# Performance work log

Measured on AMD Instinct MI355X. Metric: run time of the kernel, lower is better.

## Reference

```python
import jax, jax.numpy as jnp
import numpy as np

N = 8192        # number of cells/nodes
D_IN = 30       # input feature dim
P_DIM = 3       # position dim
HID = 32        # attention hidden dim
D_OUT = 30      # backbone output dim
FF = 128        # MLP hidden width
SIGMA = 0.3     # spatial decay sigma


def setup_inputs() -> dict:
    key = jax.random.key(0)
    ks = jax.random.split(key, 12)
    w = lambda k, shape: (jax.random.normal(k, shape, jnp.float32) * 0.1)
    return {
        "t": jax.random.uniform(ks[0], (1,), jnp.float32),
        "Z": jax.random.normal(ks[1], (N, D_IN + P_DIM + 1), jnp.float32),
        # SpatialAttentionLayer params (Q/K/V projections + output proj)
        "Wq": w(ks[2], (D_IN, HID)), "bq": jnp.zeros((HID,), jnp.float32),
        "Wk": w(ks[3], (D_IN, HID)), "bk": jnp.zeros((HID,), jnp.float32),
        "Wv": w(ks[4], (D_IN, HID)), "bv": jnp.zeros((HID,), jnp.float32),
        "Wo": w(ks[5], (HID, D_OUT)), "bo": jnp.zeros((D_OUT,), jnp.float32),
        # LayerNorm
        "ln_g": jnp.ones((D_OUT,), jnp.float32), "ln_b": jnp.zeros((D_OUT,), jnp.float32),
        # backbone MLP: Linear(30,128) -> SiLU -> Linear(128,30)
        "W1": w(ks[6], (D_OUT, FF)), "b1": jnp.zeros((FF,), jnp.float32),
        "W2": w(ks[7], (FF, D_OUT)), "b2": jnp.zeros((D_OUT,), jnp.float32),
        # expr_head: Linear(30,30)
        "We": w(ks[8], (D_OUT, D_OUT)), "be": jnp.zeros((D_OUT,), jnp.float32),
    }


def reference(t, Z, Wq, bq, Wk, bk, Wv, bv, Wo, bo, ln_g, ln_b, W1, b1, W2, b2, We, be):
    # Z: (N, D_IN + P_DIM + 1); last column is kinetic energy (unused in fwd)
    X = Z[:, :-1]                       # (N, 33)
    P = X[:, -P_DIM:]                   # (N, 3) positions
    F = X[:, :D_IN]                     # (N, 30) features

    # --- SpatialAttentionLayer: sigma distance-decay attention, no softmax ---
    Q = F @ Wq + bq
    K = F @ Wk + bk
    V = F @ Wv + bv
    scores = (Q @ K.T) / jnp.sqrt(jnp.float32(HID))          # (N, N)
    pn = jnp.sum(P * P, axis=1)
    d2 = jnp.maximum(pn[:, None] + pn[None, :] - 2.0 * (P @ P.T), 0.0)
    decay = jnp.exp(-d2 / (2.0 * SIGMA * SIGMA))              # spatial decay kernel
    A = jax.nn.sigmoid(scores) * decay                        # no-softmax attention
    A = A / (jnp.sum(A, axis=1, keepdims=True) + 1e-8)        # row-normalized message passing
    H = (A @ V) @ Wo + bo                                     # (N, D_OUT)

    # --- LayerNorm(output_dim) ---
    mu = jnp.mean(H, axis=-1, keepdims=True)
    var = jnp.mean((H - mu) ** 2, axis=-1, keepdims=True)
    Hn = (H - mu) * jax.lax.rsqrt(var + 1e-5) * ln_g + ln_b

    # --- Linear(30,128) -> SiLU -> Linear(128,30) ---
    H2 = jax.nn.silu(Hn @ W1 + b1) @ W2 + b2

    # --- expr_head ---
    feature_velo = H2 @ We + be                               # (N, 30)

    # static_pos=True -> zero position velocities (velocity_head bypassed)
    pos_velo = jnp.zeros_like(P)                              # (N, 3)

    # kinetic energy term
    ke = 0.5 * jnp.mean(feature_velo ** 2, axis=1) + 0.5 * jnp.mean(pos_velo ** 2, axis=1)
    return jnp.concatenate([feature_velo, pos_velo, ke[:, None]], axis=1)  # (N, 34)
```

## Files before the change

kernel.cpp:

```cpp
#include <hip/hip_runtime.h>
#include <hip/hip_bf16.h>

#define N      8192
#define D_IN   30
#define HID    32
#define D_OUT  30
#define FFD    128
#define ZC     34

typedef __attribute__((ext_vector_type(8))) short short8;
typedef __attribute__((ext_vector_type(16))) float f32x16;
typedef __attribute__((ext_vector_type(2))) float f32x2;

static __device__ __forceinline__ ushort f2bf(float x) {
    uint32_t u = __float_as_uint(x);
    uint32_t r = (u + 0x7fffu + ((u >> 16) & 1u)) >> 16;
    return (ushort)r;
}
static __device__ __forceinline__ float bf2f(ushort u) {
    return __uint_as_float(((uint32_t)u) << 16);
}

__global__ __launch_bounds__(256) void dv_qkv_kernel(
    const float* __restrict__ Z,
    const float* __restrict__ Wq, const float* __restrict__ bq,
    const float* __restrict__ Wk, const float* __restrict__ bk,
    const float* __restrict__ Wv, const float* __restrict__ bv,
    const float* __restrict__ W2, const float* __restrict__ We,
    const float* __restrict__ b2, const float* __restrict__ be,
    ushort* __restrict__ Qb, ushort* __restrict__ Kb,
    ushort* __restrict__ Vt, ushort* __restrict__ KA,
    ushort* __restrict__ QB, float* __restrict__ W2e, float* __restrict__ b2e)
{
    __shared__ ushort sv[8][33];
    const int t = blockIdx.x * 256 + threadIdx.x;
    const int i = t >> 5;
    const int h = t & 31;
    const float* z = Z + (size_t)i * ZC;

    float q = bq[h], k = bk[h], v = bv[h];
#pragma unroll
    for (int d = 0; d < D_IN; ++d) {
        float zf = z[d];
        q = fmaf(zf, Wq[d * HID + h], q);
        k = fmaf(zf, Wk[d * HID + h], k);
        v = fmaf(zf, Wv[d * HID + h], v);
    }
    const float QS = 0.17677669529663687f * 1.4426950408889634f;
    Qb[(size_t)i * HID + h] = f2bf(q * QS);
    Kb[(size_t)i * HID + h] = f2bf(k);
    sv[threadIdx.x >> 5][h] = f2bf(v);

    if (h == 0) {
        float p0 = z[D_IN], p1 = z[D_IN + 1], p2 = z[D_IN + 2];
        const float C2 = 1.4426950408889634f / 0.18f;
        const float SC = sqrtf(2.0f * C2);
        float px = p0 * SC, py = p1 * SC, pz = p2 * SC;
        float w  = -C2 * (p0 * p0 + p1 * p1 + p2 * p2);
        ushort phx = f2bf(px), phy = f2bf(py), phz = f2bf(pz);
        ushort plx = f2bf(px - bf2f(phx));
        ushort ply = f2bf(py - bf2f(phy));
        ushort plz = f2bf(pz - bf2f(phz));
        ushort wh  = f2bf(w);
        ushort wl  = f2bf(w - bf2f(wh));
        const ushort one = 0x3F80;
        ushort ka0[8] = {wh, wl, one, one, phx, phy, phz, phx};
        ushort ka1[8] = {phy, phz, plx, ply, plz, plx, ply, plz};
        ushort qb0[8] = {one, one, wh, wl, phx, phy, phz, plx};
        ushort qb1[8] = {ply, plz, phx, phy, phz, plx, ply, plz};
        *(uint4*)&KA[(size_t)i * 8]           = *(uint4*)ka0;
        *(uint4*)&KA[((size_t)N + i) * 8]     = *(uint4*)ka1;
        *(uint4*)&QB[(size_t)i * 8]           = *(uint4*)qb0;
        *(uint4*)&QB[((size_t)N + i) * 8]     = *(uint4*)qb1;
    }

    if (blockIdx.x < 15) {
        int idx = blockIdx.x * 256 + threadIdx.x;
        int f = idx / 30, o = idx - f * 30;
        float acc = 0.f;
#pragma unroll
        for (int d = 0; d < D_OUT; ++d)
            acc = fmaf(W2[f * D_OUT + d], We[d * D_OUT + o], acc);
        W2e[idx] = acc;
        if (idx < D_OUT) {
            float a2 = be[idx];
#pragma unroll
            for (int d = 0; d < D_OUT; ++d)
                a2 = fmaf(b2[d], We[d * D_OUT + idx], a2);
            b2e[idx] = a2;
        }
    }

    __syncthreads();
    const int ho = threadIdx.x >> 3, io = threadIdx.x & 7;
    const int i0 = blockIdx.x * 8;
    Vt[(size_t)ho * N + i0 + io] = sv[io][ho];
}

__global__ __launch_bounds__(256, 2) void dv_attn_kernel(
    const ushort* __restrict__ Qb, const ushort* __restrict__ Kb,
    const ushort* __restrict__ Vt, const ushort* __restrict__ KA,
    const ushort* __restrict__ QB, float* __restrict__ partial, int nch)
{
    __shared__ ushort lK[128 * 32];
    __shared__ ushort lV[32 * 128];
    __shared__ ushort lKA[2][128 * 8];

    const int tid  = threadIdx.x;
    const int lane = tid & 63;
    const int wv   = tid >> 6;
    const int h2   = lane >> 5;
    const int l31  = lane & 31;
    const int rb   = blockIdx.x & 63;
    const int jg   = blockIdx.x >> 6;
    const int i0w  = rb * 128 + wv * 32;

    const ushort* qp = Qb + (size_t)(i0w + l31) * HID + h2 * 8;
    const short8 qf0 = *(const short8*)qp;
    const short8 qf1 = *(const short8*)(qp + 16);
    const short8 qaug = *(const short8*)&QB[((size_t)h2 * N + i0w + l31) * 8];

    f32x16 zacc, oacc;
#pragma unroll
    for (int r = 0; r < 16; ++r) { zacc[r] = 0.f; oacc[r] = 0.f; }
    float ssA = 0.f, ssB = 0.f;

    const int cA0 = (h2 + (l31 >> 1)) & 3;
    const int cA1 = (cA0 + 2) & 3;

    for (int ch = 0; ch < nch; ++ch) {
        const int j0 = (jg * nch + ch) << 7;
        __syncthreads();
        {
            int idx = tid;
#pragma unroll
            for (int rep = 0; rep < 2; ++rep, idx += 256) {
                int jr = idx >> 2, c = idx & 3;
                int c2 = (c + (jr >> 1)) & 3;
                *(uint4*)&lK[jr * 32 + c2 * 8] =
                    *(const uint4*)&Kb[(size_t)(j0 + jr) * HID + c * 8];
            }
            idx = tid;
#pragma unroll
            for (int rep = 0; rep < 4; ++rep, idx += 256) {
                int hh = idx >> 5, cc = idx & 31;
                int cs = cc ^ hh;
                *(uint2*)&lV[hh * 128 + cs * 4] =
                    *(const uint2*)&Vt[(size_t)hh * N + j0 + cc * 4];
            }
            {
                int half = tid >> 7, jj = tid & 127;
                *(uint4*)&lKA[half][jj * 8] =
                    *(const uint4*)&KA[((size_t)half * N + j0 + jj) * 8];
            }
        }
        __syncthreads();

#pragma unroll
        for (int t32 = 0; t32 < 4; ++t32) {
            const ushort* krow = &lK[(t32 * 32 + l31) * 32];
            short8 kf0 = *(const short8*)&krow[cA0 * 8];
            short8 kf1 = *(const short8*)&krow[cA1 * 8];
            f32x16 s = __builtin_amdgcn_mfma_f32_32x32x16_bf16(kf0, qf0, zacc, 0, 0, 0);
            s = __builtin_amdgcn_mfma_f32_32x32x16_bf16(kf1, qf1, s, 0, 0, 0);

            short8 kaug = *(const short8*)&lKA[h2][(t32 * 32 + l31) * 8];
            f32x16 gA = __builtin_amdgcn_mfma_f32_32x32x16_bf16(kaug, qaug, zacc, 0, 0, 0);

            uint32_t pk[8];
#pragma unroll
            for (int p = 0; p < 8; ++p) {
                float g0 = fminf(gA[2 * p], 0.f);
                float g1 = fminf(gA[2 * p + 1], 0.f);
                float eg0 = __builtin_amdgcn_exp2f(g0);
                float es0 = __builtin_amdgcn_exp2f(-s[2 * p]);
                float a0  = eg0 * __builtin_amdgcn_rcpf(1.0f + es0);
                float eg1 = __builtin_amdgcn_exp2f(g1);
                float es1 = __builtin_amdgcn_exp2f(-s[2 * p + 1]);
                float a1  = eg1 * __builtin_amdgcn_rcpf(1.0f + es1);
                ssA += a0;
                ssB += a1;
                asm("v_cvt_pk_bf16_f32 %0, %1, %2" : "=v"(pk[p]) : "v"(a0), "v"(a1));
            }
            union BV { uint32_t u[4]; short8 v; };
            BV fa, fb;
            fa.u[0] = pk[0]; fa.u[1] = pk[1]; fa.u[2] = pk[2]; fa.u[3] = pk[3];
            fb.u[0] = pk[4]; fb.u[1] = pk[5]; fb.u[2] = pk[6]; fb.u[3] = pk[7];

            const ushort* vrow = &lV[l31 * 128];
            const int cb = t32 * 8 + h2;
            BV b0, b1;
            *(uint2*)&b0.u[0] = *(const uint2*)&vrow[((cb    ) ^ l31) * 4];
            *(uint2*)&b0.u[2] = *(const uint2*)&vrow[((cb + 2) ^ l31) * 4];
            *(uint2*)&b1.u[0] = *(const uint2*)&vrow[((cb + 4) ^ l31) * 4];
            *(uint2*)&b1.u[2] = *(const uint2*)&vrow[((cb + 6) ^ l31) * 4];

            oacc = __builtin_amdgcn_mfma_f32_32x32x16_bf16(fa.v, b0.v, oacc, 0, 0, 0);
            oacc = __builtin_amdgcn_mfma_f32_32x32x16_bf16(fb.v, b1.v, oacc, 0, 0, 0);
        }
    }

    float ssum = ssA + ssB;
    float sst = ssum + __shfl_xor(ssum, 32, 64);
    const size_t pbase = (size_t)jg * N * 33;
    if (lane < 32)
        partial[pbase + (size_t)(i0w + lane) * 33 + 32] = sst;
#pragma unroll
    for (int r = 0; r < 16; ++r) {
        int ir = (r & 3) + 8 * (r >> 2) + 4 * h2 + i0w;
        partial[pbase + (size_t)ir * 33 + l31] = oacc[r];
    }
}

__global__ __launch_bounds__(256) void dv_epilogue_kernel(
    const float* __restrict__ partial, int JG,
    const float* __restrict__ Wo, const float* __restrict__ bo,
    const float* __restrict__ ln_g, const float* __restrict__ ln_b,
    const float* __restrict__ W1, const float* __restrict__ b1,
    const float* __restrict__ W2e, const float* __restrict__ b2e,
    float* __restrict__ out)
{
    __shared__ float sr [33 * 16];
    __shared__ float sHl[30 * 16];
    __shared__ float sHn[30 * 16];
    __shared__ float shf[128 * 16];
    __shared__ float sker[16 * 16];

    const int tid  = threadIdx.x;
    const int row0 = blockIdx.x * 16;

    for (int idx = tid; idx < 33 * 16; idx += 256) {
        int r = idx / 33, c = idx - r * 33;
        const float* pp = partial + (size_t)(row0 + r) * 33 + c;
        float s = 0.f;
#pragma unroll 4
        for (int jg = 0; jg < JG; ++jg)
            s += pp[(size_t)jg * N * 33];
        sr[c * 16 + r] = s;
    }
    __syncthreads();

    const int rl  = tid & 15, grp = tid >> 4;
    const int o0  = grp * 2;
    const bool g15 = grp < 15;

    if (g15) {
        float a0 = 0.f, a1 = 0.f;
#pragma unroll
        for (int h = 0; h < HID; ++h) {
            float2 w = *(const float2*)&Wo[h * D_OUT + o0];
            float sc = sr[h * 16 + rl];
            a0 = fmaf(sc, w.x, a0); a1 = fmaf(sc, w.y, a1);
        }
        float inv = __builtin_amdgcn_rcpf(sr[32 * 16 + rl] + 1e-8f);
        float2 bb = *(const float2*)&bo[o0];
        sHl[(o0    ) * 16 + rl] = fmaf(a0, inv, bb.x);
        sHl[(o0 + 1) * 16 + rl] = fmaf(a1, inv, bb.y);
    }
    __syncthreads();

    if (tid < 16) {
        const int r = tid;
        float mu = 0.f;
#pragma unroll
        for (int o = 0; o < D_OUT; ++o) mu += sHl[o * 16 + r];
        mu *= (1.0f / D_OUT);
        float var = 0.f;
#pragma unroll
        for (int o = 0; o < D_OUT; ++o) {
            float d = sHl[o * 16 + r] - mu; var = fmaf(d, d, var);
        }
        float rs = rsqrtf(var * (1.0f / D_OUT) + 1e-5f);
#pragma unroll
        for (int o = 0; o < D_OUT; ++o)
            sHn[o * 16 + r] = fmaf((sHl[o * 16 + r] - mu) * rs, ln_g[o], ln_b[o]);
    }
    __syncthreads();

    {
        const int f0 = grp * 8;
        float acc[8];
        float4 b4a = *(const float4*)&b1[f0];
        float4 b4b = *(const float4*)&b1[f0 + 4];
        acc[0] = b4a.x; acc[1] = b4a.y; acc[2] = b4a.z; acc[3] = b4a.w;
        acc[4] = b4b.x; acc[5] = b4b.y; acc[6] = b4b.z; acc[7] = b4b.w;
#pragma unroll
        for (int o = 0; o < D_OUT; ++o) {
            float4 wa = *(const float4*)&W1[o * FFD + f0];
            float4 wb = *(const float4*)&W1[o * FFD + f0 + 4];
            float hn = sHn[o * 16 + rl];
            acc[0] = fmaf(hn, wa.x, acc[0]); acc[1] = fmaf(hn, wa.y, acc[1]);
            acc[2] = fmaf(hn, wa.z, acc[2]); acc[3] = fmaf(hn, wa.w, acc[3]);
            acc[4] = fmaf(hn, wb.x, acc[4]); acc[5] = fmaf(hn, wb.y, acc[5]);
            acc[6] = fmaf(hn, wb.z, acc[6]); acc[7] = fmaf(hn, wb.w, acc[7]);
        }
        const float L2E = 1.4426950408889634f;
#pragma unroll
        for (int ff = 0; ff < 8; ++ff) {
            float a = acc[ff];
            shf[(f0 + ff) * 16 + rl] =
                a * __builtin_amdgcn_rcpf(1.0f + __builtin_amdgcn_exp2f(-a * L2E));
        }
    }
    __syncthreads();

    if (g15) {
        float2 bb = *(const float2*)&b2e[o0];
        float a0 = bb.x, a1 = bb.y;
#pragma unroll 8
        for (int f = 0; f < FFD; ++f) {
            float2 w = *(const float2*)&W2e[f * D_OUT + o0];
            float hf = shf[f * 16 + rl];
            a0 = fmaf(hf, w.x, a0); a1 = fmaf(hf, w.y, a1);
        }
        float* op = out + (size_t)(row0 + rl) * ZC;
        op[o0] = a0; op[o0 + 1] = a1;
        sker[grp * 16 + rl] = fmaf(a0, a0, a1 * a1);
    }
    __syncthreads();

    if (tid < 16) {
        float ke = 0.f;
#pragma unroll
        for (int g = 0; g < 15; ++g) ke += sker[g * 16 + tid];
        float* op = out + (size_t)(row0 + tid) * ZC;
        op[30] = 0.f; op[31] = 0.f; op[32] = 0.f;
        op[33] = ke * (0.5f / D_OUT);
    }
}

extern "C" void kernel_launch(void* const* d_in, const int* in_sizes, int n_in,
                              void* d_out, int out_size, void* d_ws, size_t ws_size,
                              hipStream_t stream)
{
    const float* Z  = (const float*)d_in[1];
    const float* Wq = (const float*)d_in[2];
    const float* bq = (const float*)d_in[3];
    const float* Wk = (const float*)d_in[4];
    const float* bk = (const float*)d_in[5];
    const float* Wv = (const float*)d_in[6];
    const float* bv = (const float*)d_in[7];
    const float* Wo = (const float*)d_in[8];
    const float* bo = (const float*)d_in[9];
    const float* lg = (const float*)d_in[10];
    const float* lb = (const float*)d_in[11];
    const float* W1 = (const float*)d_in[12];
    const float* b1 = (const float*)d_in[13];
    const float* W2 = (const float*)d_in[14];
    const float* b2 = (const float*)d_in[15];
    const float* We = (const float*)d_in[16];
    const float* be = (const float*)d_in[17];
    float* out = (float*)d_out;

    ushort* Qb = (ushort*)d_ws;
    ushort* Kb = Qb + (size_t)N * HID;
    ushort* Vt = Kb + (size_t)N * HID;
    ushort* KA = Vt + (size_t)N * HID;
    ushort* QB = KA + (size_t)N * 16;
    float* W2e = (float*)(QB + (size_t)N * 16);
    float* b2e = W2e + FFD * D_OUT;
    float* partial = b2e + 32;

    size_t base_bytes = (size_t)((char*)partial - (char*)d_ws);
    int JG = 16;
    while (JG > 1 && base_bytes + (size_t)JG * N * 33 * 4 > ws_size) JG >>= 1;
    int nch = N / (JG * 128);

    hipLaunchKernelGGL(dv_qkv_kernel, dim3((N * HID) / 256), dim3(256), 0, stream,
                       Z, Wq, bq, Wk, bk, Wv, bv, W2, We, b2, be,
                       Qb, Kb, Vt, KA, QB, W2e, b2e);
    hipLaunchKernelGGL(dv_attn_kernel, dim3(64 * JG), dim3(256), 0, stream,
                       Qb, Kb, Vt, KA, QB, partial, nch);
    hipLaunchKernelGGL(dv_epilogue_kernel, dim3(N / 16), dim3(256), 0, stream,
                       partial, JG, Wo, bo, lg, lb, W1, b1, W2e, b2e, out);
}
```

Before: 66.85 us.

## Fold Wo into V and compute row sums via a ones column in the MFMA

The QKV kernel now precomputes V·Wo (30 columns) plus a constant ones column, stored transposed as bf16. The attention kernel therefore gets the row-normalizer from the matrix product and drops its per-element scalar sum accumulation. The partial buffer is laid out row-major with JG contiguous, which makes the epilogue reduction coalesced and removes the Wo matmul there. The decay sign is folded into the augmented K operand. Row sums now come from bf16-rounded A values, and JG is fixed at 16 with no check against workspace size.

```diff
diff --git a/kernel.cpp b/kernel.cpp
--- a/kernel.cpp
+++ b/kernel.cpp
@@ -7,10 +7,10 @@
 #define D_OUT  30
 #define FFD    128
 #define ZC     34
+#define JGC    16
 
 typedef __attribute__((ext_vector_type(8))) short short8;
 typedef __attribute__((ext_vector_type(16))) float f32x16;
-typedef __attribute__((ext_vector_type(2))) float f32x2;
 
 static __device__ __forceinline__ ushort f2bf(float x) {
     uint32_t u = __float_as_uint(x);
@@ -26,10 +26,11 @@
     const float* __restrict__ Wq, const float* __restrict__ bq,
     const float* __restrict__ Wk, const float* __restrict__ bk,
     const float* __restrict__ Wv, const float* __restrict__ bv,
+    const float* __restrict__ Wo,
     const float* __restrict__ W2, const float* __restrict__ We,
     const float* __restrict__ b2, const float* __restrict__ be,
     ushort* __restrict__ Qb, ushort* __restrict__ Kb,
-    ushort* __restrict__ Vt, ushort* __restrict__ KA,
+    ushort* __restrict__ VWot, ushort* __restrict__ KA,
     ushort* __restrict__ QB, float* __restrict__ W2e, float* __restrict__ b2e)
 {
     __shared__ ushort sv[8][33];
@@ -63,15 +64,18 @@
         ushort plz = f2bf(pz - bf2f(phz));
         ushort wh  = f2bf(w);
         ushort wl  = f2bf(w - bf2f(wh));
-        const ushort one = 0x3F80;
-        ushort ka0[8] = {wh, wl, one, one, phx, phy, phz, phx};
-        ushort ka1[8] = {phy, phz, plx, ply, plz, plx, ply, plz};
+        ushort nhx = phx ^ 0x8000, nhy = phy ^ 0x8000, nhz = phz ^ 0x8000;
+        ushort nlx = plx ^ 0x8000, nly = ply ^ 0x8000, nlz = plz ^ 0x8000;
+        ushort nwh = wh ^ 0x8000,  nwl = wl ^ 0x8000;
+        const ushort one = 0x3F80, none = 0xBF80;
+        ushort ka0[8] = {nwh, nwl, none, none, nhx, nhy, nhz, nhx};
+        ushort ka1[8] = {nhy, nhz, nlx, nly, nlz, nlx, nly, nlz};
         ushort qb0[8] = {one, one, wh, wl, phx, phy, phz, plx};
         ushort qb1[8] = {ply, plz, phx, phy, phz, plx, ply, plz};
-        *(uint4*)&KA[(size_t)i * 8]           = *(uint4*)ka0;
-        *(uint4*)&KA[((size_t)N + i) * 8]     = *(uint4*)ka1;
-        *(uint4*)&QB[(size_t)i * 8]           = *(uint4*)qb0;
-        *(uint4*)&QB[((size_t)N + i) * 8]     = *(uint4*)qb1;
+        *(uint4*)&KA[(size_t)i * 8]       = *(uint4*)ka0;
+        *(uint4*)&KA[((size_t)N + i) * 8] = *(uint4*)ka1;
+        *(uint4*)&QB[(size_t)i * 8]       = *(uint4*)qb0;
+        *(uint4*)&QB[((size_t)N + i) * 8] = *(uint4*)qb1;
     }
 
     if (blockIdx.x < 15) {
@@ -92,14 +96,24 @@
     }
 
     __syncthreads();
-    const int ho = threadIdx.x >> 3, io = threadIdx.x & 7;
-    const int i0 = blockIdx.x * 8;
-    Vt[(size_t)ho * N + i0 + io] = sv[io][ho];
+    const int io = threadIdx.x >> 5, c = threadIdx.x & 31;
+    const int ii = blockIdx.x * 8 + io;
+    float val;
+    if (c < 30) {
+        float acc = 0.f;
+#pragma unroll
+        for (int hh = 0; hh < HID; ++hh)
+            acc = fmaf(bf2f(sv[io][hh]), Wo[hh * D_OUT + c], acc);
+        val = acc;
+    } else {
+        val = (c == 31) ? 1.0f : 0.f;
+    }
+    VWot[(size_t)c * N + ii] = f2bf(val);
 }
 
 __global__ __launch_bounds__(256, 2) void dv_attn_kernel(
     const ushort* __restrict__ Qb, const ushort* __restrict__ Kb,
-    const ushort* __restrict__ Vt, const ushort* __restrict__ KA,
+    const ushort* __restrict__ VWot, const ushort* __restrict__ KA,
     const ushort* __restrict__ QB, float* __restrict__ partial, int nch)
 {
     __shared__ ushort lK[128 * 32];
@@ -123,7 +137,6 @@
     f32x16 zacc, oacc;
 #pragma unroll
     for (int r = 0; r < 16; ++r) { zacc[r] = 0.f; oacc[r] = 0.f; }
-    float ssA = 0.f, ssB = 0.f;
 
     const int cA0 = (h2 + (l31 >> 1)) & 3;
     const int cA1 = (cA0 + 2) & 3;
@@ -135,10 +148,10 @@
             int idx = tid;
 #pragma unroll
             for (int rep = 0; rep < 2; ++rep, idx += 256) {
-                int jr = idx >> 2, c = idx & 3;
-                int c2 = (c + (jr >> 1)) & 3;
+                int jr = idx >> 2, cc = idx & 3;
+                int c2 = (cc + (jr >> 1)) & 3;
                 *(uint4*)&lK[jr * 32 + c2 * 8] =
-                    *(const uint4*)&Kb[(size_t)(j0 + jr) * HID + c * 8];
+                    *(const uint4*)&Kb[(size_t)(j0 + jr) * HID + cc * 8];
             }
             idx = tid;
 #pragma unroll
@@ -146,7 +159,7 @@
                 int hh = idx >> 5, cc = idx & 31;
                 int cs = cc ^ hh;
                 *(uint2*)&lV[hh * 128 + cs * 4] =
-                    *(const uint2*)&Vt[(size_t)hh * N + j0 + cc * 4];
+                    *(const uint2*)&VWot[(size_t)hh * N + j0 + cc * 4];
             }
             {
                 int half = tid >> 7, jj = tid & 127;
@@ -170,16 +183,14 @@
             uint32_t pk[8];
 #pragma unroll
             for (int p = 0; p < 8; ++p) {
-                float g0 = fminf(gA[2 * p], 0.f);
-                float g1 = fminf(gA[2 * p + 1], 0.f);
-                float eg0 = __builtin_amdgcn_exp2f(g0);
+                float d0 = fmaxf(gA[2 * p], 0.f);
+                float d1 = fmaxf(gA[2 * p + 1], 0.f);
+                float eg0 = __builtin_amdgcn_exp2f(-d0);
                 float es0 = __builtin_amdgcn_exp2f(-s[2 * p]);
                 float a0  = eg0 * __builtin_amdgcn_rcpf(1.0f + es0);
-                float eg1 = __builtin_amdgcn_exp2f(g1);
+                float eg1 = __builtin_amdgcn_exp2f(-d1);
                 float es1 = __builtin_amdgcn_exp2f(-s[2 * p + 1]);
                 float a1  = eg1 * __builtin_amdgcn_rcpf(1.0f + es1);
-                ssA += a0;
-                ssB += a1;
                 asm("v_cvt_pk_bf16_f32 %0, %1, %2" : "=v"(pk[p]) : "v"(a0), "v"(a1));
             }
             union BV { uint32_t u[4]; short8 v; };
@@ -200,27 +211,22 @@
         }
     }
 
-    float ssum = ssA + ssB;
-    float sst = ssum + __shfl_xor(ssum, 32, 64);
-    const size_t pbase = (size_t)jg * N * 33;
-    if (lane < 32)
-        partial[pbase + (size_t)(i0w + lane) * 33 + 32] = sst;
 #pragma unroll
     for (int r = 0; r < 16; ++r) {
         int ir = (r & 3) + 8 * (r >> 2) + 4 * h2 + i0w;
-        partial[pbase + (size_t)ir * 33 + l31] = oacc[r];
+        partial[(size_t)ir * (JGC * 32) + jg * 32 + l31] = oacc[r];
     }
 }
 
 __global__ __launch_bounds__(256) void dv_epilogue_kernel(
-    const float* __restrict__ partial, int JG,
-    const float* __restrict__ Wo, const float* __restrict__ bo,
+    const float* __restrict__ partial,
+    const float* __restrict__ bo,
     const float* __restrict__ ln_g, const float* __restrict__ ln_b,
     const float* __restrict__ W1, const float* __restrict__ b1,
     const float* __restrict__ W2e, const float* __restrict__ b2e,
     float* __restrict__ out)
 {
-    __shared__ float sr [33 * 16];
+    __shared__ float sr [32 * 16];
     __shared__ float sHl[30 * 16];
     __shared__ float sHn[30 * 16];
     __shared__ float shf[128 * 16];
@@ -229,13 +235,15 @@
     const int tid  = threadIdx.x;
     const int row0 = blockIdx.x * 16;
 
-    for (int idx = tid; idx < 33 * 16; idx += 256) {
-        int r = idx / 33, c = idx - r * 33;
-        const float* pp = partial + (size_t)(row0 + r) * 33 + c;
+#pragma unroll
+    for (int rep = 0; rep < 2; ++rep) {
+        int idx = tid + rep * 256;
+        int r = idx >> 5, c = idx & 31;
+        const float* pp = partial + (size_t)(row0 + r) * (JGC * 32) + c;
         float s = 0.f;
-#pragma unroll 4
-        for (int jg = 0; jg < JG; ++jg)
-            s += pp[(size_t)jg * N * 33];
+#pragma unroll
+        for (int jg = 0; jg < JGC; ++jg)
+            s += pp[jg * 32];
         sr[c * 16 + r] = s;
     }
     __syncthreads();
@@ -245,17 +253,10 @@
     const bool g15 = grp < 15;
 
     if (g15) {
-        float a0 = 0.f, a1 = 0.f;
-#pragma unroll
-        for (int h = 0; h < HID; ++h) {
-            float2 w = *(const float2*)&Wo[h * D_OUT + o0];
-            float sc = sr[h * 16 + rl];
-            a0 = fmaf(sc, w.x, a0); a1 = fmaf(sc, w.y, a1);
-        }
-        float inv = __builtin_amdgcn_rcpf(sr[32 * 16 + rl] + 1e-8f);
+        float inv = __builtin_amdgcn_rcpf(sr[31 * 16 + rl] + 1e-8f);
         float2 bb = *(const float2*)&bo[o0];
-        sHl[(o0    ) * 16 + rl] = fmaf(a0, inv, bb.x);
-        sHl[(o0 + 1) * 16 + rl] = fmaf(a1, inv, bb.y);
+        sHl[(o0    ) * 16 + rl] = fmaf(sr[(o0    ) * 16 + rl], inv, bb.x);
+        sHl[(o0 + 1) * 16 + rl] = fmaf(sr[(o0 + 1) * 16 + rl], inv, bb.y);
     }
     __syncthreads();
 
@@ -352,25 +353,22 @@
     const float* be = (const float*)d_in[17];
     float* out = (float*)d_out;
 
-    ushort* Qb = (ushort*)d_ws;
-    ushort* Kb = Qb + (size_t)N * HID;
-    ushort* Vt = Kb + (size_t)N * HID;
-    ushort* KA = Vt + (size_t)N * HID;
-    ushort* QB = KA + (size_t)N * 16;
-    float* W2e = (float*)(QB + (size_t)N * 16);
-    float* b2e = W2e + FFD * D_OUT;
-    float* partial = b2e + 32;
-
-    size_t base_bytes = (size_t)((char*)partial - (char*)d_ws);
-    int JG = 16;
-    while (JG > 1 && base_bytes + (size_t)JG * N * 33 * 4 > ws_size) JG >>= 1;
-    int nch = N / (JG * 128);
+    ushort* Qb   = (ushort*)d_ws;
+    ushort* Kb   = Qb + (size_t)N * HID;
+    ushort* VWot = Kb + (size_t)N * HID;
+    ushort* KA   = VWot + (size_t)N * HID;
+    ushort* QB   = KA + (size_t)N * 16;
+    float*  W2e  = (float*)(QB + (size_t)N * 16);
+    float*  b2e  = W2e + FFD * D_OUT;
+    float*  partial = b2e + 32;
+
+    int nch = N / (JGC * 128);
 
     hipLaunchKernelGGL(dv_qkv_kernel, dim3((N * HID) / 256), dim3(256), 0, stream,
-                       Z, Wq, bq, Wk, bk, Wv, bv, W2, We, b2, be,
-                       Qb, Kb, Vt, KA, QB, W2e, b2e);
-    hipLaunchKernelGGL(dv_attn_kernel, dim3(64 * JG), dim3(256), 0, stream,
-                       Qb, Kb, Vt, KA, QB, partial, nch);
+                       Z, Wq, bq, Wk, bk, Wv, bv, Wo, W2, We, b2, be,
+                       Qb, Kb, VWot, KA, QB, W2e, b2e);
+    hipLaunchKernelGGL(dv_attn_kernel, dim3(64 * JGC), dim3(256), 0, stream,
+                       Qb, Kb, VWot, KA, QB, partial, nch);
     hipLaunchKernelGGL(dv_epilogue_kernel, dim3(N / 16), dim3(256), 0, stream,
-                       partial, JG, Wo, bo, lg, lb, W1, b1, W2e, b2e, out);
-}
+                       partial, bo, lg, lb, W1, b1, W2e, b2e, out);
+}
```

Result: faster. 63.85 us (-4.5%).
